# Kernel optimization log

Hardware: AMD Instinct MI355X
Metric: run time of the kernel (lower is better)

The kernel has to match this reference:

```python
import jax, jax.numpy as jnp
import numpy as np

TEMPERATURE = 0.07
BASE_TEMPERATURE = 0.07


def setup_inputs() -> dict:
    key = jax.random.key(0)
    k1, k2 = jax.random.split(key)
    N, D = 8192, 512
    features = jax.random.normal(k1, (N, D), dtype=jnp.float32)
    labels = jax.random.randint(k2, (N,), 0, 64, dtype=jnp.int64 if jax.config.jax_enable_x64 else jnp.int32)
    return {"features": features, "labels": labels, "rotation_multiplier": 2}


def reference(features, labels, rotation_multiplier):
    k = int(rotation_multiplier)
    N = features.shape[0]
    B = N // k
    # L2-normalize rows (torch F.normalize clamps norm at eps=1e-12)
    norm = jnp.maximum(jnp.linalg.norm(features, axis=1, keepdims=True), 1e-12)
    f = features / norm
    sim = jnp.matmul(f, f.T) / TEMPERATURE  # [N, N]

    # block positive mask: groups of k rows share a label; compare group labels
    lab = labels.reshape(B, k)[:, 0]  # [B]
    same = lab[:, None] == lab[None, :]  # [B, B]
    mask = jnp.repeat(jnp.repeat(same, k, axis=0), k, axis=1)  # [N, N]
    eye = jnp.eye(N, dtype=bool)
    mask = mask & ~eye

    # stable masked log-softmax with diagonal removed from denominator
    logits_max = jax.lax.stop_gradient(jnp.max(sim, axis=1, keepdims=True))
    logits = sim - logits_max
    exp_logits = jnp.exp(logits)
    denom = exp_logits.sum(axis=1, keepdims=True) - jnp.diagonal(exp_logits)[:, None] + 1e-8
    log_prob = logits - jnp.log(denom)

    mask_f = mask.astype(logits.dtype)
    mask_sum = mask_f.sum(axis=1)  # [N]
    valid = mask_sum > 0
    mean_log_prob_pos = (log_prob * mask_f).sum(axis=1) / jnp.maximum(mask_sum, 1.0)
    per_sample = -(TEMPERATURE / BASE_TEMPERATURE) * mean_log_prob_pos
    n_valid = valid.sum().astype(logits.dtype)
    loss = jnp.where(valid, per_sample, 0.0).sum() / jnp.maximum(n_valid, 1.0)
    return loss
```

## Files before the change

### kernel.cpp

```cpp
#include <hip/hip_runtime.h>
#include <hip/hip_bf16.h>

#define TEMP_INV 14.285714285714286f
#define FSCALE 16.0f
#define T1S (TEMP_INV / 256.0f)
#define NSLICE 16

typedef __attribute__((ext_vector_type(4))) float f32x4;
typedef __attribute__((ext_vector_type(4))) int i32x4;
typedef __attribute__((ext_vector_type(8))) int i32x8;


__global__ __launch_bounds__(256) void norm_k(const float* __restrict__ feat,
                                              uchar* __restrict__ fq,
                                              const int* __restrict__ labels,
                                              const int* __restrict__ kptr,
                                              int* __restrict__ glab,
                                              float* __restrict__ gacc,
                                              int* __restrict__ dcnt,
                                              int N, int D) {
  const int row = (blockIdx.x * 256 + threadIdx.x) >> 6;
  const int lane = threadIdx.x & 63;
  if (row < N) {
    const float4* fr = (const float4*)(feat + (size_t)row * D);
    float4 v0 = fr[lane * 2];
    float4 v1 = fr[lane * 2 + 1];
    float ss = v0.x * v0.x + v0.y * v0.y + v0.z * v0.z + v0.w * v0.w +
               v1.x * v1.x + v1.y * v1.y + v1.z * v1.z + v1.w * v1.w;
    #pragma unroll
    for (int off = 32; off; off >>= 1) ss += __shfl_xor(ss, off, 64);
    const float inv = FSCALE / fmaxf(sqrtf(ss), 1e-12f);
    int w0 = 0, w1 = 0;
    w0 = __builtin_amdgcn_cvt_pk_fp8_f32(v0.x * inv, v0.y * inv, w0, false);
    w0 = __builtin_amdgcn_cvt_pk_fp8_f32(v0.z * inv, v0.w * inv, w0, true);
    w1 = __builtin_amdgcn_cvt_pk_fp8_f32(v1.x * inv, v1.y * inv, w1, false);
    w1 = __builtin_amdgcn_cvt_pk_fp8_f32(v1.z * inv, v1.w * inv, w1, true);
    uint2 o; o.x = (uint)w0; o.y = (uint)w1;
    const int tkb  = lane >> 4;
    const int quad = (lane >> 2) & 3;
    const int half = (lane >> 1) & 1;
    const int slot = half * 64 + quad * 16 + (row & 15);
    uchar* dstp = fq + (((size_t)(row >> 4) * (D >> 7) + tkb) << 11) +
                  slot * 16 + (lane & 1) * 8;
    *(uint2*)dstp = o;
    if (lane == 0) {
      const int k = *kptr;
      glab[row] = labels[(size_t)(row / k) * k];
    }
  }
  if (blockIdx.x == 0 && threadIdx.x < 3) {
    if (threadIdx.x < 2) gacc[threadIdx.x] = 0.f;
    else *dcnt = 0;
  }
}

__global__ __launch_bounds__(128) void gemm_k(const uchar* __restrict__ fq,
                                              const int* __restrict__ glab,
                                              float* __restrict__ partS,
                                              float* __restrict__ partP,
                                              int N, int D) {
  const int lane = threadIdx.x & 63;
  const int wid  = threadIdx.x >> 6;
  const int quad = lane >> 4, l15 = lane & 15;
  const int ktiles = D >> 7;
  const int strip = (int)(blockIdx.x / NSLICE) * 2 + wid;
  const int slice = (int)(blockIdx.x % NSLICE);
  const int r0 = strip * 32;
  const int cps = N / NSLICE;
  const int jsteps = cps >> 6;
  const int j0base = slice * cps;

  int rlab[2][4];
  #pragma unroll
  for (int mi = 0; mi < 2; mi++)
    #pragma unroll
    for (int r = 0; r < 4; r++)
      rlab[mi][r] = glab[r0 + mi * 16 + quad * 4 + r];

  float Srun[2][4] = {{0.f, 0.f, 0.f, 0.f}, {0.f, 0.f, 0.f, 0.f}};
  float Prun[2][4] = {{0.f, 0.f, 0.f, 0.f}, {0.f, 0.f, 0.f, 0.f}};

#define LOADF(dst, grp, kt)                                                   \
  {                                                                           \
    const uchar* p_ = fq + (((size_t)((grp) * ktiles + (kt))) << 11) + lane * 16; \
    i32x4 lo_ = *(const i32x4*)p_;                                            \
    i32x4 hi_ = *(const i32x4*)(p_ + 1024);                                   \
    dst = (i32x8){lo_.x, lo_.y, lo_.z, lo_.w, hi_.x, hi_.y, hi_.z, hi_.w};    \
  }

#define EPILOG(j0)                                                            \
  {                                                                           \
    int clab[4];                                                              \
    _Pragma("unroll")                                                         \
    for (int ni = 0; ni < 4; ni++) clab[ni] = glab[(j0) + ni * 16 + l15];     \
    _Pragma("unroll")                                                         \
    for (int mi = 0; mi < 2; mi++)                                            \
      _Pragma("unroll")                                                       \
      for (int r = 0; r < 4; r++) {                                           \
        const int row = r0 + mi * 16 + quad * 4 + r;                          \
        const int rl = rlab[mi][r];                                           \
        float s = 0.f, pp = 0.f;                                              \
        _Pragma("unroll")                                                     \
        for (int ni = 0; ni < 4; ni++) {                                      \
          const int col = (j0) + ni * 16 + l15;                               \
          const float lg = fmaf(acc[mi][ni][r], T1S, -TEMP_INV);              \
          const bool diag = (col == row);                                     \
          s += diag ? 0.f : __expf(lg);                                       \
          pp += (!diag && rl == clab[ni]) ? lg : 0.f;                         \
        }                                                                     \
        Srun[mi][r] += s;                                                     \
        Prun[mi][r] += pp;                                                    \
      }                                                                       \
  }

  if (ktiles == 4) {
    i32x8 af[2][4];
    #pragma unroll
    for (int mi = 0; mi < 2; mi++)
      #pragma unroll
      for (int kt = 0; kt < 4; kt++)
        LOADF(af[mi][kt], (r0 >> 4) + mi, kt)

    for (int js = 0; js < jsteps; js++) {
      const int j0 = j0base + js * 64;
      f32x4 acc[2][4];
      #pragma unroll
      for (int mi = 0; mi < 2; mi++)
        #pragma unroll
        for (int ni = 0; ni < 4; ni++) {
          f32x4 z = {0.f, 0.f, 0.f, 0.f};
          acc[mi][ni] = z;
        }
      #pragma unroll
      for (int kt = 0; kt < 4; kt++) {
        i32x8 bv[4];
        #pragma unroll
        for (int ni = 0; ni < 4; ni++)
          LOADF(bv[ni], (j0 >> 4) + ni, kt)
        #pragma unroll
        for (int mi = 0; mi < 2; mi++)
          #pragma unroll
          for (int ni = 0; ni < 4; ni++)
            acc[mi][ni] = __builtin_amdgcn_mfma_scale_f32_16x16x128_f8f6f4(
                af[mi][kt], bv[ni], acc[mi][ni], 0, 0, 0, 127, 0, 127);
      }
      EPILOG(j0)
    }
  } else {
    for (int js = 0; js < jsteps; js++) {
      const int j0 = j0base + js * 64;
      f32x4 acc[2][4];
      #pragma unroll
      for (int mi = 0; mi < 2; mi++)
        #pragma unroll
        for (int ni = 0; ni < 4; ni++) {
          f32x4 z = {0.f, 0.f, 0.f, 0.f};
          acc[mi][ni] = z;
        }
      for (int kt = 0; kt < ktiles; kt++) {
        i32x8 as[2], bv[4];
        #pragma unroll
        for (int mi = 0; mi < 2; mi++) LOADF(as[mi], (r0 >> 4) + mi, kt)
        #pragma unroll
        for (int ni = 0; ni < 4; ni++) LOADF(bv[ni], (j0 >> 4) + ni, kt)
        #pragma unroll
        for (int mi = 0; mi < 2; mi++)
          #pragma unroll
          for (int ni = 0; ni < 4; ni++)
            acc[mi][ni] = __builtin_amdgcn_mfma_scale_f32_16x16x128_f8f6f4(
                as[mi], bv[ni], acc[mi][ni], 0, 0, 0, 127, 0, 127);
      }
      EPILOG(j0)
    }
  }
#undef LOADF
#undef EPILOG

  #pragma unroll
  for (int mi = 0; mi < 2; mi++)
    #pragma unroll
    for (int r = 0; r < 4; r++) {
      float s = Srun[mi][r], p = Prun[mi][r];
      #pragma unroll
      for (int off = 1; off < 16; off <<= 1) {
        s += __shfl_xor(s, off, 64);
        p += __shfl_xor(p, off, 64);
      }
      if (l15 == 0) {
        const int row = r0 + mi * 16 + quad * 4 + r;
        partS[(size_t)row * NSLICE + slice] = s;
        partP[(size_t)row * NSLICE + slice] = p;
      }
    }
}

__global__ __launch_bounds__(256) void reduce_loss_k(const float* __restrict__ partS,
                                                     const float* __restrict__ partP,
                                                     const int* __restrict__ glab,
                                                     const int* __restrict__ labels,
                                                     const int* __restrict__ kptr,
                                                     float* __restrict__ gacc,
                                                     int* __restrict__ dcnt,
                                                     float* __restrict__ out, int N) {
  const int tt = threadIdx.x;
  const int row = blockIdx.x * 256 + tt;
  const int k = *kptr;
  const int B = N / k;

  __shared__ int h[64];
  if (tt < 64) h[tt] = 0;
  __syncthreads();
  for (int g = tt; g < B; g += 256) {
    int lb = labels[(size_t)g * k];
    if (lb >= 0 && lb < 64) atomicAdd(&h[lb], 1);
  }
  __syncthreads();

  float l = 0.f, v = 0.f;
  if (row < N) {
    float S = 0.f, P = 0.f;
    #pragma unroll
    for (int s = 0; s < NSLICE; s++) {
      S += partS[(size_t)row * NSLICE + s];
      P += partP[(size_t)row * NSLICE + s];
    }
    const int np = h[glab[row]] * k - 1;
    if (np > 0) {
      l = -(P - (float)np * logf(S + 1e-8f)) / (float)np;
      v = 1.f;
    }
  }
  #pragma unroll
  for (int off = 32; off; off >>= 1) {
    l += __shfl_xor(l, off, 64);
    v += __shfl_xor(v, off, 64);
  }
  __shared__ float sl4[4], sv4[4];
  if ((tt & 63) == 0) { sl4[tt >> 6] = l; sv4[tt >> 6] = v; }
  __syncthreads();
  if (tt == 0) {
    float L = 0.f, V = 0.f;
    #pragma unroll
    for (int i = 0; i < 4; i++) { L += sl4[i]; V += sv4[i]; }
    atomicAdd(&gacc[0], L);
    atomicAdd(&gacc[1], V);
    __threadfence();
    const int prev = atomicAdd(dcnt, 1);
    if (prev == (int)gridDim.x - 1) {
      const float Lf = atomicAdd(&gacc[0], 0.f);
      const float Vf = atomicAdd(&gacc[1], 0.f);
      out[0] = Lf / fmaxf(Vf, 1.f);
    }
  }
}

extern "C" void kernel_launch(void* const* d_in, const int* in_sizes, int n_in,
                              void* d_out, int out_size, void* d_ws, size_t ws_size,
                              hipStream_t stream) {
  const float* feat = (const float*)d_in[0];
  const int* labels = (const int*)d_in[1];
  const int* kptr   = (const int*)d_in[2];
  const int N = in_sizes[1];
  const int D = in_sizes[0] / N;

  char* ws = (char*)d_ws;
  uchar* fq = (uchar*)ws;
  size_t off = (size_t)N * D;
  float* partS = (float*)(ws + off); off += (size_t)N * NSLICE * sizeof(float);
  float* partP = (float*)(ws + off); off += (size_t)N * NSLICE * sizeof(float);
  int* glab    = (int*)(ws + off);   off += (size_t)N * sizeof(int);
  float* gacc  = (float*)(ws + off); off += 2 * sizeof(float);
  int* dcnt    = (int*)(ws + off);   off += sizeof(int);

  const int strips = N / 32;
  const int ggrid = (strips / 2) * NSLICE;

  norm_k<<<(N + 3) / 4, 256, 0, stream>>>(feat, fq, labels, kptr, glab,
                                          gacc, dcnt, N, D);
  gemm_k<<<ggrid, 128, 0, stream>>>(fq, glab, partS, partP, N, D);
  reduce_loss_k<<<(N + 255) / 256, 256, 0, stream>>>(partS, partP, glab, labels,
                                                     kptr, gacc, dcnt,
                                                     (float*)d_out, N);
}
```

Before: 132.0 us.

## Double-buffer B-fragment loads across k-tiles and halve column slices in fused GEMM

Replaces the per-k-tile load-then-MFMA loop with two alternating sets of B-fragment registers, so the next k-tile (and the next column block's first tile) is prefetched while the current MFMAs run. It also cuts the column slices from 16 to 8, which halves the grid and the partial-sum traffic but gives each wave twice as many column steps. A launch-bounds occupancy hint is added. The extra live registers may reduce occupancy, and the smaller grid gives less parallelism.

```diff
diff --git a/kernel.cpp b/kernel.cpp
--- a/kernel.cpp
+++ b/kernel.cpp
@@ -4,7 +4,6 @@
 #define TEMP_INV 14.285714285714286f
 #define FSCALE 16.0f
 #define T1S (TEMP_INV / 256.0f)
-#define NSLICE 16
 
 typedef __attribute__((ext_vector_type(4))) float f32x4;
 typedef __attribute__((ext_vector_type(4))) int i32x4;
@@ -54,19 +53,19 @@
   }
 }
 
-__global__ __launch_bounds__(128) void gemm_k(const uchar* __restrict__ fq,
-                                              const int* __restrict__ glab,
-                                              float* __restrict__ partS,
-                                              float* __restrict__ partP,
-                                              int N, int D) {
+__global__ __launch_bounds__(128, 2) void gemm_k(const uchar* __restrict__ fq,
+                                                 const int* __restrict__ glab,
+                                                 float* __restrict__ partS,
+                                                 float* __restrict__ partP,
+                                                 int N, int D) {
   const int lane = threadIdx.x & 63;
   const int wid  = threadIdx.x >> 6;
   const int quad = lane >> 4, l15 = lane & 15;
   const int ktiles = D >> 7;
-  const int strip = (int)(blockIdx.x / NSLICE) * 2 + wid;
-  const int slice = (int)(blockIdx.x % NSLICE);
+  const int strip = (blockIdx.x >> 3) * 2 + wid;
+  const int slice = blockIdx.x & 7;
   const int r0 = strip * 32;
-  const int cps = N / NSLICE;
+  const int cps = N >> 3;
   const int jsteps = cps >> 6;
   const int j0base = slice * cps;
 
@@ -83,9 +82,26 @@
 #define LOADF(dst, grp, kt)                                                   \
   {                                                                           \
     const uchar* p_ = fq + (((size_t)((grp) * ktiles + (kt))) << 11) + lane * 16; \
-    i32x4 lo_ = *(const i32x4*)p_;                                            \
-    i32x4 hi_ = *(const i32x4*)(p_ + 1024);                                   \
-    dst = (i32x8){lo_.x, lo_.y, lo_.z, lo_.w, hi_.x, hi_.y, hi_.z, hi_.w};    \
+    i32x4* d_ = (i32x4*)&(dst);                                               \
+    d_[0] = *(const i32x4*)p_;                                                \
+    d_[1] = *(const i32x4*)(p_ + 1024);                                       \
+  }
+
+#define LOADB4(B0, B1, B2, B3, j0, kt)                                        \
+  LOADF(B0, ((j0) >> 4) + 0, kt) LOADF(B1, ((j0) >> 4) + 1, kt)               \
+  LOADF(B2, ((j0) >> 4) + 2, kt) LOADF(B3, ((j0) >> 4) + 3, kt)
+
+#define MFMA8(B0, B1, B2, B3, kt)                                             \
+  _Pragma("unroll")                                                           \
+  for (int mi = 0; mi < 2; mi++) {                                            \
+    acc[mi][0] = __builtin_amdgcn_mfma_scale_f32_16x16x128_f8f6f4(            \
+        af[mi][kt], B0, acc[mi][0], 0, 0, 0, 127, 0, 127);                    \
+    acc[mi][1] = __builtin_amdgcn_mfma_scale_f32_16x16x128_f8f6f4(            \
+        af[mi][kt], B1, acc[mi][1], 0, 0, 0, 127, 0, 127);                    \
+    acc[mi][2] = __builtin_amdgcn_mfma_scale_f32_16x16x128_f8f6f4(            \
+        af[mi][kt], B2, acc[mi][2], 0, 0, 0, 127, 0, 127);                    \
+    acc[mi][3] = __builtin_amdgcn_mfma_scale_f32_16x16x128_f8f6f4(            \
+        af[mi][kt], B3, acc[mi][3], 0, 0, 0, 127, 0, 127);                    \
   }
 
 #define EPILOG(j0)                                                            \
@@ -121,6 +137,9 @@
       for (int kt = 0; kt < 4; kt++)
         LOADF(af[mi][kt], (r0 >> 4) + mi, kt)
 
+    i32x8 bX0, bX1, bX2, bX3, bY0, bY1, bY2, bY3;
+    LOADB4(bX0, bX1, bX2, bX3, j0base, 0)
+
     for (int js = 0; js < jsteps; js++) {
       const int j0 = j0base + js * 64;
       f32x4 acc[2][4];
@@ -131,19 +150,16 @@
           f32x4 z = {0.f, 0.f, 0.f, 0.f};
           acc[mi][ni] = z;
         }
-      #pragma unroll
-      for (int kt = 0; kt < 4; kt++) {
-        i32x8 bv[4];
-        #pragma unroll
-        for (int ni = 0; ni < 4; ni++)
-          LOADF(bv[ni], (j0 >> 4) + ni, kt)
-        #pragma unroll
-        for (int mi = 0; mi < 2; mi++)
-          #pragma unroll
-          for (int ni = 0; ni < 4; ni++)
-            acc[mi][ni] = __builtin_amdgcn_mfma_scale_f32_16x16x128_f8f6f4(
-                af[mi][kt], bv[ni], acc[mi][ni], 0, 0, 0, 127, 0, 127);
+      LOADB4(bY0, bY1, bY2, bY3, j0, 1)
+      MFMA8(bX0, bX1, bX2, bX3, 0)
+      LOADB4(bX0, bX1, bX2, bX3, j0, 2)
+      MFMA8(bY0, bY1, bY2, bY3, 1)
+      LOADB4(bY0, bY1, bY2, bY3, j0, 3)
+      MFMA8(bX0, bX1, bX2, bX3, 2)
+      if (js + 1 < jsteps) {
+        LOADB4(bX0, bX1, bX2, bX3, j0 + 64, 0)
       }
+      MFMA8(bY0, bY1, bY2, bY3, 3)
       EPILOG(j0)
     }
   } else {
@@ -158,22 +174,26 @@
           acc[mi][ni] = z;
         }
       for (int kt = 0; kt < ktiles; kt++) {
-        i32x8 as[2], bv[4];
+        i32x8 af[2][4];
+        LOADF(af[0][0], (r0 >> 4) + 0, kt)
+        LOADF(af[1][0], (r0 >> 4) + 1, kt)
+        i32x8 bv[4];
         #pragma unroll
-        for (int mi = 0; mi < 2; mi++) LOADF(as[mi], (r0 >> 4) + mi, kt)
-        #pragma unroll
-        for (int ni = 0; ni < 4; ni++) LOADF(bv[ni], (j0 >> 4) + ni, kt)
+        for (int ni = 0; ni < 4; ni++)
+          LOADF(bv[ni], (j0 >> 4) + ni, kt)
         #pragma unroll
         for (int mi = 0; mi < 2; mi++)
           #pragma unroll
           for (int ni = 0; ni < 4; ni++)
             acc[mi][ni] = __builtin_amdgcn_mfma_scale_f32_16x16x128_f8f6f4(
-                as[mi], bv[ni], acc[mi][ni], 0, 0, 0, 127, 0, 127);
+                af[mi][0], bv[ni], acc[mi][ni], 0, 0, 0, 127, 0, 127);
       }
       EPILOG(j0)
     }
   }
 #undef LOADF
+#undef LOADB4
+#undef MFMA8
 #undef EPILOG
 
   #pragma unroll
@@ -188,8 +208,8 @@
       }
       if (l15 == 0) {
         const int row = r0 + mi * 16 + quad * 4 + r;
-        partS[(size_t)row * NSLICE + slice] = s;
-        partP[(size_t)row * NSLICE + slice] = p;
+        partS[(size_t)row * 8 + slice] = s;
+        partP[(size_t)row * 8 + slice] = p;
       }
     }
 }
@@ -220,9 +240,9 @@
   if (row < N) {
     float S = 0.f, P = 0.f;
     #pragma unroll
-    for (int s = 0; s < NSLICE; s++) {
-      S += partS[(size_t)row * NSLICE + s];
-      P += partP[(size_t)row * NSLICE + s];
+    for (int s = 0; s < 8; s++) {
+      S += partS[(size_t)row * 8 + s];
+      P += partP[(size_t)row * 8 + s];
     }
     const int np = h[glab[row]] * k - 1;
     if (np > 0) {
@@ -266,14 +286,14 @@
   char* ws = (char*)d_ws;
   uchar* fq = (uchar*)ws;
   size_t off = (size_t)N * D;
-  float* partS = (float*)(ws + off); off += (size_t)N * NSLICE * sizeof(float);
-  float* partP = (float*)(ws + off); off += (size_t)N * NSLICE * sizeof(float);
+  float* partS = (float*)(ws + off); off += (size_t)N * 8 * sizeof(float);
+  float* partP = (float*)(ws + off); off += (size_t)N * 8 * sizeof(float);
   int* glab    = (int*)(ws + off);   off += (size_t)N * sizeof(int);
   float* gacc  = (float*)(ws + off); off += 2 * sizeof(float);
   int* dcnt    = (int*)(ws + off);   off += sizeof(int);
 
   const int strips = N / 32;
-  const int ggrid = (strips / 2) * NSLICE;
+  const int ggrid = (strips / 2) * 8;
 
   norm_k<<<(N + 3) / 4, 256, 0, stream>>>(feat, fq, labels, kptr, glab,
                                           gacc, dcnt, N, D);
```

Result: slower. 156.4 us (+18.4%).
